# Kernel tuning notes

Hardware: AMD Instinct MI355X
Metric: run time of the kernel (lower is better)

## Reference

```python
import jax, jax.numpy as jnp
import numpy as np

B, L = 8, 512
D_MODEL, N_HEADS, N_LAYERS = 768, 12, 12
D_HEAD = D_MODEL // N_HEADS
D_FF = 4 * D_MODEL
NUM_LABELS = 1000
PATCH_DIM = 16 * 16 * 3
EPS = 1e-6


def setup_inputs() -> dict:
    key = jax.random.key(0)
    ks = jax.random.split(key, 24)
    d = D_MODEL

    def w(k, shape, fan_in):
        return (jax.random.normal(k, shape, jnp.float32) / np.sqrt(fan_in)).astype(jnp.float32)

    return {
        'patch': jax.random.normal(ks[0], (B, L, PATCH_DIM), jnp.float32),
        'box': jax.random.uniform(ks[1], (B, L, 4), jnp.float32),
        'patch_W': w(ks[2], (PATCH_DIM, d), PATCH_DIM),
        'patch_b': jnp.zeros((d,), jnp.float32),
        'box_W': w(ks[3], (d, d), d),
        'box_b': jnp.zeros((d,), jnp.float32),
        'Wq': w(ks[4], (N_LAYERS, d, d), d),
        'Wk': w(ks[5], (N_LAYERS, d, d), d),
        'Wv': w(ks[6], (N_LAYERS, d, d), d),
        'Wo': w(ks[7], (N_LAYERS, d, d), d),
        'attn_norm_w': jnp.ones((N_LAYERS, d), jnp.float32),
        'gate_W': w(ks[8], (N_LAYERS, d, D_FF), d),
        'hidden_W': w(ks[9], (N_LAYERS, d, D_FF), d),
        'ffn_out_W': w(ks[10], (N_LAYERS, D_FF, d), D_FF),
        'ffn_norm_w': jnp.ones((N_LAYERS, d), jnp.float32),
        'reward_norm_w': jnp.ones((d,), jnp.float32),
        'reward_W': w(ks[11], (d, 2), d),
        'reward_b': jnp.zeros((2,), jnp.float32),
        'label_norm_w': jnp.ones((d,), jnp.float32),
        'label_W': w(ks[12], (d, NUM_LABELS), d),
        'label_b': jnp.zeros((NUM_LABELS,), jnp.float32),
        'box_norm_w': jnp.ones((d,), jnp.float32),
        'boxh_W': w(ks[13], (d, 4), d),
        'boxh_b': jnp.zeros((4,), jnp.float32),
    }


def _rmsnorm(x, wgt):
    return x * jax.lax.rsqrt(jnp.mean(x * x, axis=-1, keepdims=True) + EPS) * wgt


def _rope(x, cos, sin):
    # x: [b, n, l, dh]; consecutive pairs form complex numbers (view_as_complex)
    xr, xi = x[..., 0::2], x[..., 1::2]
    out_r = xr * cos - xi * sin
    out_i = xr * sin + xi * cos
    return jnp.stack((out_r, out_i), axis=-1).reshape(x.shape)


def _forward(patch, box, patch_W, patch_b, box_W, box_b, Wq, Wk, Wv, Wo,
             attn_norm_w, gate_W, hidden_W, ffn_out_W, ffn_norm_w,
             reward_norm_w, reward_W, reward_b, label_norm_w, label_W, label_b,
             box_norm_w, boxh_W, boxh_b):
    b, l, _ = patch.shape
    d = D_MODEL
    # StackedSinusoidalEmbedding(d_model, 4): d_stack = d/4, theta over d_stack/2 freqs
    d_stack = d // 4
    theta_box = 1.0 / (10000.0 ** (2.0 * jnp.arange(d_stack // 2, dtype=jnp.float32) / d_stack))
    ang = box[..., None] * theta_box  # [b, l, 4, d_stack/2]
    box_sin = jnp.stack((jnp.cos(ang), jnp.sin(ang)), axis=-1).reshape(b, l, d)

    x = (patch @ patch_W + patch_b) + (box_sin @ box_W + box_b)

    # RoPE tables and causal mask (constants)
    theta = 1.0 / (10000.0 ** (2.0 * jnp.arange(D_HEAD // 2, dtype=jnp.float32) / D_HEAD))
    pos_ang = jnp.arange(l, dtype=jnp.float32)[:, None] * theta  # [l, dh/2]
    cos, sin = jnp.cos(pos_ang), jnp.sin(pos_ang)
    mask = jnp.triu(jnp.full((l, l), -jnp.inf, dtype=jnp.float32), 1)
    scale = jnp.float32(np.sqrt(D_HEAD))

    def block(h, p):
        wq, wk, wv, wo, anw, gw, hw, ow, fnw = p
        hn = _rmsnorm(h, anw)
        q = (hn @ wq).reshape(b, l, N_HEADS, D_HEAD).transpose(0, 2, 1, 3)
        k = (hn @ wk).reshape(b, l, N_HEADS, D_HEAD).transpose(0, 2, 1, 3)
        v = (hn @ wv).reshape(b, l, N_HEADS, D_HEAD).transpose(0, 2, 1, 3)
        scores = jnp.einsum('bnld,bnmd->bnlm', _rope(q, cos, sin), _rope(k, cos, sin)) / scale
        attn = jax.nn.softmax(scores + mask, axis=-1)
        o = jnp.einsum('bnlm,bnmd->bnld', attn, v).transpose(0, 2, 1, 3).reshape(b, l, d)
        h = h + o @ wo
        hn = _rmsnorm(h, fnw)
        h = h + (jax.nn.silu(hn @ gw) * (hn @ hw)) @ ow
        return h, None

    x, _ = jax.lax.scan(block, x, (Wq, Wk, Wv, Wo, attn_norm_w, gate_W, hidden_W, ffn_out_W, ffn_norm_w))

    reward = _rmsnorm(x, reward_norm_w) @ reward_W + reward_b
    label = _rmsnorm(x, label_norm_w) @ label_W + label_b
    box_out = _rmsnorm(x, box_norm_w) @ boxh_W + boxh_b
    return reward, label, box_out


def reference(patch, box, patch_W, patch_b, box_W, box_b, Wq, Wk, Wv, Wo,
              attn_norm_w, gate_W, hidden_W, ffn_out_W, ffn_norm_w,
              reward_norm_w, reward_W, reward_b, label_norm_w, label_W, label_b,
              box_norm_w, boxh_W, boxh_b):
    return _forward(patch, box, patch_W, patch_b, box_W, box_b, Wq, Wk, Wv, Wo,
                    attn_norm_w, gate_W, hidden_W, ffn_out_W, ffn_norm_w,
                    reward_norm_w, reward_W, reward_b, label_norm_w, label_W, label_b,
                    box_norm_w, boxh_W, boxh_b)
```

## Files before the change

### kernel.cpp

```cpp
#include <hip/hip_runtime.h>
#include <math.h>
#include <type_traits>

#define B_   8
#define L_   512
#define MTOK 4096
#define D_   768
#define NH_  12
#define DH_  64
#define DFF_ 3072
#define NL_  12

typedef unsigned short u16;
typedef __attribute__((ext_vector_type(4))) float f32x4;
typedef __attribute__((ext_vector_type(8))) short i16x8;
typedef __attribute__((ext_vector_type(8))) __bf16 b16x8;

template <typename A, typename = void>
struct PickFrag { using type = i16x8; };
template <typename A>
struct PickFrag<A, std::void_t<decltype(__builtin_amdgcn_mfma_f32_16x16x32_bf16(
    std::declval<A>(), std::declval<A>(), std::declval<f32x4>(), 0, 0, 0))>> {
  using type = A;
};
using frag_t = typename PickFrag<b16x8>::type;

#if __has_builtin(__builtin_amdgcn_global_load_lds)
#define HAS_GLDS 1
#else
#define HAS_GLDS 0
#endif

__device__ inline u16 f2bf(float f) {
    unsigned u = __float_as_uint(f);
    unsigned r = u + 0x7fffu + ((u >> 16) & 1u);
    return (u16)(r >> 16);
}
__device__ inline float bf2f(u16 b) { return __uint_as_float(((unsigned)b) << 16); }

__device__ inline void bar_raw() {
    asm volatile("" ::: "memory");
    __builtin_amdgcn_s_barrier();
    asm volatile("" ::: "memory");
}

__device__ inline int swz8(int row, int c8) { return c8 ^ ((row & 7) << 3); }

__global__ void k_box_sin(u16* __restrict__ emb, const float* __restrict__ box) {
    int idx = blockIdx.x * blockDim.x + threadIdx.x;
    if (idx >= MTOK * D_) return;
    int t = idx / D_, d = idx % D_;
    int c = d / 192, r = d % 192, j = r >> 1;
    float theta = __expf(-(float)j * (9.210340371976184f / 96.0f));
    float ang = box[t * 4 + c] * theta;
    emb[(size_t)t * 1536 + 768 + d] = f2bf((r & 1) ? sinf(ang) : cosf(ang));
}

__global__ void k_cast(u16* __restrict__ emb, const float* __restrict__ in, int n4) {
    int i = blockIdx.x * blockDim.x + threadIdx.x;
    if (i >= n4) return;
    int t = i / 192, c4 = (i % 192) * 4;
    float4 v = *reinterpret_cast<const float4*>(in + (size_t)t * 768 + c4);
    unsigned lo = (unsigned)f2bf(v.x) | ((unsigned)f2bf(v.y) << 16);
    unsigned hi = (unsigned)f2bf(v.z) | ((unsigned)f2bf(v.w) << 16);
    *reinterpret_cast<uint2*>(emb + (size_t)t * 1536 + c4) = make_uint2(lo, hi);
}

__global__ void k_addb(float* __restrict__ dst, const float* __restrict__ a,
                       const float* __restrict__ b) {
    int i = blockIdx.x * blockDim.x + threadIdx.x;
    if (i < D_) dst[i] = a[i] + b[i];
}

__global__ __launch_bounds__(256) void k_convT(u16* __restrict__ dst,
                                               const float* __restrict__ src,
                                               int K, int N, int ld, int rs,
                                               int ro, int co) {
    __shared__ float t[32][33];
    int bn = blockIdx.x * 32;
    int bk = blockIdx.y * 32;
    int tx = threadIdx.x % 32, ty = threadIdx.x / 32;
    #pragma unroll
    for (int i = 0; i < 4; ++i) {
        int k = bk + ty + i * 8;
        int n = bn + tx;
        t[ty + i * 8][tx] = (n < N) ? src[(size_t)k * N + n] : 0.0f;
    }
    __syncthreads();
    #pragma unroll
    for (int i = 0; i < 4; ++i) {
        int n = bn + ty + i * 8;
        int k = bk + tx;
        dst[(size_t)(n * rs + ro) * ld + co + k] = f2bf(t[tx][ty + i * 8]);
    }
}


__global__ __launch_bounds__(256) void k_convT128(u16* __restrict__ dst,
                                                  const float* __restrict__ src,
                                                  int K, int N) {
    __shared__ float ts[32][130];
    const float* s = src + (size_t)blockIdx.z * K * N;
    u16* d = dst + (size_t)blockIdx.z * K * N;
    int bn = blockIdx.x * 32, bk = blockIdx.y * 128;
    int t = threadIdx.x, rn = t & 31, kr = t >> 5;
    #pragma unroll
    for (int p = 0; p < 16; ++p) {
        int k = p * 8 + kr;
        ts[rn][k] = s[(size_t)(bk + k) * N + bn + rn];
    }
    __syncthreads();
    int n = t >> 3, kc = (t & 7) * 16;
    u16 tmp[16];
    #pragma unroll
    for (int j = 0; j < 16; ++j) tmp[j] = f2bf(ts[n][kc + j]);
    u16* dp = &d[(size_t)(bn + n) * K + bk + kc];
    *reinterpret_cast<uint4*>(dp)     = *reinterpret_cast<uint4*>(tmp);
    *reinterpret_cast<uint4*>(dp + 8) = *reinterpret_cast<uint4*>(tmp + 8);
}

__global__ __launch_bounds__(256) void k_convT128_qkv(u16* __restrict__ dst,
                                                      const float* __restrict__ s0,
                                                      const float* __restrict__ s1,
                                                      const float* __restrict__ s2) {
    __shared__ float ts[32][130];
    int ly = blockIdx.z / 3, which = blockIdx.z % 3;
    const float* s = (which == 0 ? s0 : (which == 1 ? s1 : s2)) + (size_t)ly * 768 * 768;
    u16* d = dst + ((size_t)ly * 3 + which) * 768 * 768;
    int bn = blockIdx.x * 32, bk = blockIdx.y * 128;
    int t = threadIdx.x, rn = t & 31, kr = t >> 5;
    #pragma unroll
    for (int p = 0; p < 16; ++p) {
        int k = p * 8 + kr;
        ts[rn][k] = s[(size_t)(bk + k) * 768 + bn + rn];
    }
    __syncthreads();
    int n = t >> 3, kc = (t & 7) * 16;
    u16 tmp[16];
    #pragma unroll
    for (int j = 0; j < 16; ++j) tmp[j] = f2bf(ts[n][kc + j]);
    u16* dp = &d[(size_t)(bn + n) * 768 + bk + kc];
    *reinterpret_cast<uint4*>(dp)     = *reinterpret_cast<uint4*>(tmp);
    *reinterpret_cast<uint4*>(dp + 8) = *reinterpret_cast<uint4*>(tmp + 8);
}

__global__ __launch_bounds__(256) void k_convT128_gh(u16* __restrict__ dst,
                                                     const float* __restrict__ g,
                                                     const float* __restrict__ h) {
    __shared__ float ts[32][130];
    int ly = blockIdx.z >> 1, which = blockIdx.z & 1;
    const float* s = (which ? h : g) + (size_t)ly * 768 * 3072;
    u16* d = dst + (size_t)ly * 6144 * 768;
    int bn = blockIdx.x * 32, bk = blockIdx.y * 128;
    int t = threadIdx.x, rn = t & 31, kr = t >> 5;
    #pragma unroll
    for (int p = 0; p < 16; ++p) {
        int k = p * 8 + kr;
        ts[rn][k] = s[(size_t)(bk + k) * 3072 + bn + rn];
    }
    __syncthreads();
    int n = t >> 3, kc = (t & 7) * 16;
    int ng = bn + n;
    int row = ((ng >> 4) << 5) + (ng & 15) + which * 16;
    u16 tmp[16];
    #pragma unroll
    for (int j = 0; j < 16; ++j) tmp[j] = f2bf(ts[n][kc + j]);
    u16* dp = &d[(size_t)row * 768 + bk + kc];
    *reinterpret_cast<uint4*>(dp)     = *reinterpret_cast<uint4*>(tmp);
    *reinterpret_cast<uint4*>(dp + 8) = *reinterpret_cast<uint4*>(tmp + 8);
}

__global__ __launch_bounds__(256) void k_rmsnorm(u16* __restrict__ out,
                                                 const float* __restrict__ in,
                                                 const float* __restrict__ w) {
    int t = blockIdx.x;
    const float* x = in + (size_t)t * D_;
    float ss = 0.f;
    for (int i = threadIdx.x; i < D_; i += 256) { float v = x[i]; ss += v * v; }
    for (int off = 32; off > 0; off >>= 1) ss += __shfl_down(ss, off);
    __shared__ float red[4];
    int wid = threadIdx.x >> 6, lane = threadIdx.x & 63;
    if (lane == 0) red[wid] = ss;
    __syncthreads();
    float tot = red[0] + red[1] + red[2] + red[3];
    float inv = rsqrtf(tot / (float)D_ + 1e-6f);
    for (int i = threadIdx.x; i < D_; i += 256)
        out[(size_t)t * D_ + i] = f2bf(x[i] * inv * w[i]);
}

template <int S>
__global__ __launch_bounds__(256) void k_fused_rr(float* __restrict__ h,
                                                  const float* __restrict__ part,
                                                  u16* __restrict__ hn,
                                                  const float* __restrict__ w) {
    int t = blockIdx.x;
    size_t base = (size_t)t * D_;
    float x[3];
    float ss = 0.f;
    #pragma unroll
    for (int c = 0; c < 3; ++c) {
        int i = threadIdx.x + c * 256;
        float v = h[base + i];
        #pragma unroll
        for (int s = 0; s < S; ++s)
            v += part[(size_t)s * MTOK * D_ + base + i];
        x[c] = v;
        h[base + i] = v;
        ss += v * v;
    }
    for (int off = 32; off > 0; off >>= 1) ss += __shfl_down(ss, off);
    __shared__ float red[4];
    int wid = threadIdx.x >> 6, lane = threadIdx.x & 63;
    if (lane == 0) red[wid] = ss;
    __syncthreads();
    float tot = red[0] + red[1] + red[2] + red[3];
    float inv = rsqrtf(tot / (float)D_ + 1e-6f);
    #pragma unroll
    for (int c = 0; c < 3; ++c) {
        int i = threadIdx.x + c * 256;
        hn[base + i] = f2bf(x[c] * inv * w[i]);
    }
}

__global__ void k_rope_tab(float* __restrict__ tab) {
    int idx = blockIdx.x * blockDim.x + threadIdx.x;
    if (idx >= L_ * 32) return;
    int l = idx >> 5, j = idx & 31;
    float theta = __expf(-(float)j * (9.210340371976184f / 32.0f));
    float s, c;
    sincosf((float)l * theta, &s, &c);
    tab[idx * 2] = c;
    tab[idx * 2 + 1] = s;
}

template <int MODE>
__global__ __launch_bounds__(256) void k_gemm_bf16(void* __restrict__ Cp,
                                                   const u16* __restrict__ A,
                                                   const u16* __restrict__ BT,
                                                   const float* __restrict__ bias,
                                                   int K, int Nout, int ldC) {
    __shared__ u16 smem[16384];
    int tid = threadIdx.x;
    int wid = tid >> 6, lane = tid & 63;

    int nx = gridDim.x, ny = gridDim.y, nz = gridDim.z;
    int bid = ((blockIdx.z * ny) + blockIdx.y) * nx + blockIdx.x;
    int nwg = nx * ny * nz;
    int cpx = nwg >> 3;
    int swz = (bid & 7) * cpx + (bid >> 3);
    int sk  = swz / (nx * ny);
    int rem = swz % (nx * ny);
    int by = rem / nx, bx = rem % nx;
    int row0 = by * 128, col0 = bx * 128;
    int wr = wid >> 1, wc = wid & 1;

    int Klen = K / nz;
    int kbeg = sk * Klen;

    int c0 = wid * 128 + lane;
    int c1 = c0 + 64;
    int r0 = c0 >> 2, kc0 = (c0 & 3) * 8;
    int r1 = c1 >> 2, kc1 = (c1 & 3) * 8;
    const u16* gA0 = A  + (size_t)(row0 + r0) * K + kbeg + kc0;
    const u16* gA1 = A  + (size_t)(row0 + r1) * K + kbeg + kc1;
    const u16* gB0 = BT + (size_t)(col0 + r0) * K + kbeg + kc0;
    const u16* gB1 = BT + (size_t)(col0 + r1) * K + kbeg + kc1;

    auto stage = [&](int buf, int kt) {
        u16* Asb = smem + buf * 4096;
        u16* Bsb = smem + 8192 + buf * 4096;
#if HAS_GLDS
        __builtin_amdgcn_global_load_lds(
            (const __attribute__((address_space(1))) void*)(gA0 + kt),
            (__attribute__((address_space(3))) void*)&Asb[c0 * 8], 16, 0, 0);
        __builtin_amdgcn_global_load_lds(
            (const __attribute__((address_space(1))) void*)(gA1 + kt),
            (__attribute__((address_space(3))) void*)&Asb[c1 * 8], 16, 0, 0);
        __builtin_amdgcn_global_load_lds(
            (const __attribute__((address_space(1))) void*)(gB0 + kt),
            (__attribute__((address_space(3))) void*)&Bsb[c0 * 8], 16, 0, 0);
        __builtin_amdgcn_global_load_lds(
            (const __attribute__((address_space(1))) void*)(gB1 + kt),
            (__attribute__((address_space(3))) void*)&Bsb[c1 * 8], 16, 0, 0);
#else
        *reinterpret_cast<uint4*>(&Asb[c0 * 8]) = *reinterpret_cast<const uint4*>(gA0 + kt);
        *reinterpret_cast<uint4*>(&Asb[c1 * 8]) = *reinterpret_cast<const uint4*>(gA1 + kt);
        *reinterpret_cast<uint4*>(&Bsb[c0 * 8]) = *reinterpret_cast<const uint4*>(gB0 + kt);
        *reinterpret_cast<uint4*>(&Bsb[c1 * 8]) = *reinterpret_cast<const uint4*>(gB1 + kt);
#endif
    };

    f32x4 acc[4][4] = {};
    int lrow = lane & 15, lk = (lane >> 4) * 8;

    stage(0, 0);
    int cur = 0;
    for (int kt = 0; kt < Klen; kt += 32) {
        bool has_next = (kt + 32 < Klen);
        if (has_next) stage(cur ^ 1, kt + 32);
        if (has_next) asm volatile("s_waitcnt vmcnt(4) lgkmcnt(0)" ::: "memory");
        else          asm volatile("s_waitcnt vmcnt(0) lgkmcnt(0)" ::: "memory");
        __builtin_amdgcn_sched_barrier(0);
        bar_raw();
        const u16* Asb = smem + cur * 4096;
        const u16* Bsb = smem + 8192 + cur * 4096;
        frag_t af[4], bfr[4];
        #pragma unroll
        for (int m = 0; m < 4; ++m)
            af[m] = *reinterpret_cast<const frag_t*>(&Asb[(wr * 64 + m * 16 + lrow) * 32 + lk]);
        #pragma unroll
        for (int n = 0; n < 4; ++n)
            bfr[n] = *reinterpret_cast<const frag_t*>(&Bsb[(wc * 64 + n * 16 + lrow) * 32 + lk]);
        #pragma unroll
        for (int m = 0; m < 4; ++m)
            #pragma unroll
            for (int n = 0; n < 4; ++n)
                acc[m][n] = __builtin_amdgcn_mfma_f32_16x16x32_bf16(af[m], bfr[n], acc[m][n], 0, 0, 0);
        bar_raw();
        cur ^= 1;
    }

    int lcol = lane & 15, rb = (lane >> 4) * 4;

    if (MODE == 6) {
        u16* qkvh = (u16*)Cp;
        const float* tab = bias;
        if (col0 >= 1536) {
            int head_base = (col0 - 1536) >> 6;
            int bb = row0 >> 9;
            int l0 = row0 & 511;
            #pragma unroll
            for (int pass = 0; pass < 2; ++pass) {
                if (wc == pass) {
                    #pragma unroll
                    for (int m = 0; m < 4; ++m) {
                        #pragma unroll
                        for (int n = 0; n < 4; ++n) {
                            int dl = n * 16 + lcol;
                            int rl = wr * 64 + m * 16 + rb;
                            u16 tmp[4];
                            #pragma unroll
                            for (int e = 0; e < 4; ++e) tmp[e] = f2bf(acc[m][n][e]);
                            *reinterpret_cast<uint2*>(&smem[dl * 136 + rl]) =
                                *reinterpret_cast<uint2*>(tmp);
                        }
                    }
                }
                __syncthreads();
                int head = head_base + pass;
                size_t vbase = (size_t)2 * MTOK * 768 +
                               ((size_t)(bb * NH_ + head) * 64) * 512;
                #pragma unroll
                for (int it = 0; it < 4; ++it) {
                    int dd = it * 16 + (tid >> 4);
                    int rr = (tid & 15) * 8;
                    uint4 v4 = *reinterpret_cast<const uint4*>(&smem[dd * 136 + rr]);
                    *reinterpret_cast<uint4*>(&qkvh[vbase + (size_t)dd * 512 + l0 + rr]) = v4;
                }
                __syncthreads();
            }
        } else {
            int sec = col0 / 768;
            float qscale = (sec == 0) ? 0.125f : 1.0f;
            #pragma unroll
            for (int m = 0; m < 4; ++m) {
                #pragma unroll
                for (int n = 0; n < 4; ++n) {
                    int col = col0 + wc * 64 + n * 16 + lcol;
                    int head = (col % 768) >> 6;
                    int d = col & 63;
                    #pragma unroll
                    for (int e = 0; e < 4; ++e) {
                        int row = row0 + wr * 64 + m * 16 + rb + e;
                        int bb = row >> 9, l = row & 511;
                        float v = acc[m][n][e];
                        float p = __shfl_xor(v, 1);
                        float2 cs = *reinterpret_cast<const float2*>(
                            tab + ((size_t)l * 32 + (d >> 1)) * 2);
                        float r = (d & 1) ? (p * cs.y + v * cs.x)
                                          : (v * cs.x - p * cs.y);
                        r *= qscale;
                        qkvh[(size_t)sec * MTOK * 768 +
                             ((size_t)(bb * NH_ + head) * 512 + l) * 64 + d] = f2bf(r);
                    }
                }
            }
        }
        return;
    }

    if (MODE == 5) {
        #pragma unroll
        for (int m = 0; m < 4; ++m) {
            #pragma unroll
            for (int np = 0; np < 2; ++np) {
                int ocol = (col0 >> 1) + wc * 32 + np * 16 + lcol;
                #pragma unroll
                for (int e = 0; e < 4; ++e) {
                    int row = row0 + wr * 64 + m * 16 + rb + e;
                    float g = acc[m][2 * np][e], hv = acc[m][2 * np + 1][e];
                    float s = g / (1.0f + __expf(-g));
                    ((u16*)Cp)[(size_t)row * ldC + ocol] = f2bf(s * hv);
                }
            }
        }
        return;
    }

    float* Cpart = (MODE == 4)
        ? ((float*)Cp + (size_t)sk * (size_t)(ny * 128) * ldC) : (float*)Cp;
    #pragma unroll
    for (int m = 0; m < 4; ++m) {
        #pragma unroll
        for (int n = 0; n < 4; ++n) {
            int col = col0 + wc * 64 + n * 16 + lcol;
            if (col >= Nout) continue;
            #pragma unroll
            for (int e = 0; e < 4; ++e) {
                int row = row0 + wr * 64 + m * 16 + rb + e;
                float v = acc[m][n][e];
                size_t off = (size_t)row * ldC + col;
                if (MODE == 0) {
                    if (bias) v += bias[col];
                    ((float*)Cp)[off] = v;
                } else if (MODE == 3) {
                    ((u16*)Cp)[off] = f2bf(v);
                } else if (MODE == 4) {
                    Cpart[off] = v;
                }
            }
        }
    }
}

__global__ __launch_bounds__(256) void k_attn3(u16* __restrict__ o,
                                               const u16* __restrict__ qh,
                                               const u16* __restrict__ kh,
                                               const u16* __restrict__ vT) {
    int bh = blockIdx.x, qb = blockIdx.y;
    int b = bh / NH_, hh = bh % NH_;
    int tid = threadIdx.x, wid = tid >> 6, lane = tid & 63;
    __shared__ u16 Qs[64][72], Ps[64][72];
    __shared__ u16 Ks[64 * 64], Vs[64 * 64];

    #pragma unroll
    for (int i = 0; i < 2; ++i) {
        int idx = tid + i * 256;
        int r = idx >> 3, c8 = (idx & 7) * 8;
        uint4 v4 = *reinterpret_cast<const uint4*>(
            qh + ((size_t)bh * L_ + qb * 64 + r) * 64 + c8);
        *reinterpret_cast<uint4*>(&Qs[r][c8]) = v4;
    }
    __syncthreads();

    int lr = lane & 15, lg = lane >> 4;
    frag_t aq[2];
    #pragma unroll
    for (int kd = 0; kd < 2; ++kd)
        aq[kd] = *reinterpret_cast<const frag_t*>(&Qs[wid * 16 + lr][kd * 32 + lg * 8]);

    int sr0 = tid >> 3, sc8 = (tid & 7) * 8;
    int sr1 = sr0 + 32;

    f32x4 accO[4] = {};
    float M[4], S[4];
    #pragma unroll
    for (int e = 0; e < 4; ++e) { M[e] = -INFINITY; S[e] = 0.f; }

    uint4 kreg0 = *reinterpret_cast<const uint4*>(kh + ((size_t)bh * L_ + sr0) * 64 + sc8);
    uint4 kreg1 = *reinterpret_cast<const uint4*>(kh + ((size_t)bh * L_ + sr1) * 64 + sc8);
    uint4 vreg0 = *reinterpret_cast<const uint4*>(vT + ((size_t)bh * 64 + sr0) * L_ + sc8);
    uint4 vreg1 = *reinterpret_cast<const uint4*>(vT + ((size_t)bh * 64 + sr1) * L_ + sc8);

    for (int kb = 0; kb <= qb; ++kb) {
        __syncthreads();
        *reinterpret_cast<uint4*>(&Ks[sr0 * 64 + swz8(sr0, sc8)]) = kreg0;
        *reinterpret_cast<uint4*>(&Ks[sr1 * 64 + swz8(sr1, sc8)]) = kreg1;
        *reinterpret_cast<uint4*>(&Vs[sr0 * 64 + swz8(sr0, sc8)]) = vreg0;
        *reinterpret_cast<uint4*>(&Vs[sr1 * 64 + swz8(sr1, sc8)]) = vreg1;
        __syncthreads();
        if (kb < qb) {
            int nb = (kb + 1) * 64;
            kreg0 = *reinterpret_cast<const uint4*>(kh + ((size_t)bh * L_ + nb + sr0) * 64 + sc8);
            kreg1 = *reinterpret_cast<const uint4*>(kh + ((size_t)bh * L_ + nb + sr1) * 64 + sc8);
            vreg0 = *reinterpret_cast<const uint4*>(vT + ((size_t)bh * 64 + sr0) * L_ + nb + sc8);
            vreg1 = *reinterpret_cast<const uint4*>(vT + ((size_t)bh * 64 + sr1) * L_ + nb + sc8);
        }

        f32x4 sv[4];
        __builtin_amdgcn_s_setprio(1);
        #pragma unroll
        for (int ct = 0; ct < 4; ++ct) {
            int krow = ct * 16 + lr;
            frag_t bk0 = *reinterpret_cast<const frag_t*>(&Ks[krow * 64 + swz8(krow, lg * 8)]);
            frag_t bk1 = *reinterpret_cast<const frag_t*>(&Ks[krow * 64 + swz8(krow, 32 + lg * 8)]);
            f32x4 z = {0.f, 0.f, 0.f, 0.f};
            z = __builtin_amdgcn_mfma_f32_16x16x32_bf16(aq[0], bk0, z, 0, 0, 0);
            sv[ct] = __builtin_amdgcn_mfma_f32_16x16x32_bf16(aq[1], bk1, z, 0, 0, 0);
        }
        __builtin_amdgcn_s_setprio(0);

        bool diag = (kb == qb);
        float esc[4];
        #pragma unroll
        for (int e = 0; e < 4; ++e) {
            int qg = qb * 64 + wid * 16 + lg * 4 + e;
            float mx = -1e30f;
            #pragma unroll
            for (int ct = 0; ct < 4; ++ct) {
                float s = sv[ct][e];
                if (diag && (kb * 64 + ct * 16 + lr > qg)) s = -1e30f;
                sv[ct][e] = s;
                mx = fmaxf(mx, s);
            }
            #pragma unroll
            for (int msk = 8; msk; msk >>= 1) mx = fmaxf(mx, __shfl_xor(mx, msk));
            float newM = fmaxf(M[e], mx);
            float ps = 0.f;
            #pragma unroll
            for (int ct = 0; ct < 4; ++ct) {
                float p = __expf(sv[ct][e] - newM);
                sv[ct][e] = p;
                ps += p;
            }
            #pragma unroll
            for (int msk = 8; msk; msk >>= 1) ps += __shfl_xor(ps, msk);
            esc[e] = __expf(M[e] - newM);
            S[e] = S[e] * esc[e] + ps;
            M[e] = newM;
        }
        #pragma unroll
        for (int dt = 0; dt < 4; ++dt)
            #pragma unroll
            for (int e = 0; e < 4; ++e) accO[dt][e] *= esc[e];

        #pragma unroll
        for (int ct = 0; ct < 4; ++ct)
            #pragma unroll
            for (int e = 0; e < 4; ++e)
                Ps[wid * 16 + lg * 4 + e][ct * 16 + lr] = f2bf(sv[ct][e]);

        frag_t pa0 = *reinterpret_cast<const frag_t*>(&Ps[wid * 16 + lr][lg * 8]);
        frag_t pa1 = *reinterpret_cast<const frag_t*>(&Ps[wid * 16 + lr][32 + lg * 8]);
        __builtin_amdgcn_s_setprio(1);
        #pragma unroll
        for (int dt = 0; dt < 4; ++dt) {
            int vrow = dt * 16 + lr;
            frag_t bv0 = *reinterpret_cast<const frag_t*>(&Vs[vrow * 64 + swz8(vrow, lg * 8)]);
            frag_t bv1 = *reinterpret_cast<const frag_t*>(&Vs[vrow * 64 + swz8(vrow, 32 + lg * 8)]);
            accO[dt] = __builtin_amdgcn_mfma_f32_16x16x32_bf16(pa0, bv0, accO[dt], 0, 0, 0);
            accO[dt] = __builtin_amdgcn_mfma_f32_16x16x32_bf16(pa1, bv1, accO[dt], 0, 0, 0);
        }
        __builtin_amdgcn_s_setprio(0);
    }

    #pragma unroll
    for (int dt = 0; dt < 4; ++dt) {
        #pragma unroll
        for (int e = 0; e < 4; ++e) {
            int row = b * L_ + qb * 64 + wid * 16 + lg * 4 + e;
            o[(size_t)row * D_ + hh * 64 + dt * 16 + lr] = f2bf(accO[dt][e] / S[e]);
        }
    }
}

__global__ __launch_bounds__(256) void k_heads3(float* __restrict__ out_reward,
                                                float* __restrict__ out_box,
                                                const float* __restrict__ h,
                                                const float* __restrict__ rnw,
                                                const float* __restrict__ rW,
                                                const float* __restrict__ rb,
                                                const float* __restrict__ bnw,
                                                const float* __restrict__ bW,
                                                const float* __restrict__ bb) {
    int t = blockIdx.x;
    size_t base = (size_t)t * D_;
    float x[3];
    float ss = 0.f;
    #pragma unroll
    for (int c = 0; c < 3; ++c) {
        int i = threadIdx.x + c * 256;
        x[c] = h[base + i];
        ss += x[c] * x[c];
    }
    for (int off = 32; off > 0; off >>= 1) ss += __shfl_down(ss, off);
    __shared__ float red[4];
    int wid = threadIdx.x >> 6, lane = threadIdx.x & 63;
    if (lane == 0) red[wid] = ss;
    __syncthreads();
    float inv = rsqrtf((red[0] + red[1] + red[2] + red[3]) / (float)D_ + 1e-6f);

    float a[6] = {};
    #pragma unroll
    for (int c = 0; c < 3; ++c) {
        int i = threadIdx.x + c * 256;
        float xr = x[c] * inv;
        float xw = xr * rnw[i];
        a[0] += xw * rW[i * 2];
        a[1] += xw * rW[i * 2 + 1];
        float xb = xr * bnw[i];
        #pragma unroll
        for (int j = 0; j < 4; ++j) a[2 + j] += xb * bW[i * 4 + j];
    }
    #pragma unroll
    for (int j = 0; j < 6; ++j)
        for (int off = 32; off > 0; off >>= 1) a[j] += __shfl_down(a[j], off);
    __shared__ float red2[4][6];
    if (lane == 0)
        #pragma unroll
        for (int j = 0; j < 6; ++j) red2[wid][j] = a[j];
    __syncthreads();
    if (threadIdx.x < 6) {
        float s = red2[0][threadIdx.x] + red2[1][threadIdx.x] +
                  red2[2][threadIdx.x] + red2[3][threadIdx.x];
        if (threadIdx.x < 2) out_reward[(size_t)t * 2 + threadIdx.x] = s + rb[threadIdx.x];
        else                 out_box[(size_t)t * 4 + threadIdx.x - 2] = s + bb[threadIdx.x - 2];
    }
}

extern "C" void kernel_launch(void* const* d_in, const int* in_sizes, int n_in,
                              void* d_out, int out_size, void* d_ws, size_t ws_size,
                              hipStream_t stream) {
    const float* patch        = (const float*)d_in[0];
    const float* box          = (const float*)d_in[1];
    const float* patch_W      = (const float*)d_in[2];
    const float* patch_b      = (const float*)d_in[3];
    const float* box_W        = (const float*)d_in[4];
    const float* box_b        = (const float*)d_in[5];
    const float* Wq           = (const float*)d_in[6];
    const float* Wk           = (const float*)d_in[7];
    const float* Wv           = (const float*)d_in[8];
    const float* Wo           = (const float*)d_in[9];
    const float* attn_norm_w  = (const float*)d_in[10];
    const float* gate_W       = (const float*)d_in[11];
    const float* hidden_W     = (const float*)d_in[12];
    const float* ffn_out_W    = (const float*)d_in[13];
    const float* ffn_norm_w   = (const float*)d_in[14];
    const float* reward_norm_w= (const float*)d_in[15];
    const float* reward_W     = (const float*)d_in[16];
    const float* reward_b     = (const float*)d_in[17];
    const float* label_norm_w = (const float*)d_in[18];
    const float* label_W      = (const float*)d_in[19];
    const float* label_b      = (const float*)d_in[20];
    const float* box_norm_w   = (const float*)d_in[21];
    const float* boxh_W       = (const float*)d_in[22];
    const float* boxh_b       = (const float*)d_in[23];

    char* w = (char*)d_ws;
    auto alloc = [&](size_t bytes) { char* p = w; w += (bytes + 255) & ~(size_t)255; return p; };

    u16*  wqkv_a = (u16*)alloc((size_t)NL_ * 2304 * 768 * 2);
    u16*  wo_a   = (u16*)alloc((size_t)NL_ * 768 * 768 * 2);
    u16*  wgh_a  = (u16*)alloc((size_t)NL_ * 6144 * 768 * 2);
    u16*  wfo_a  = (u16*)alloc((size_t)NL_ * 768 * 3072 * 2);
    u16*  wcat   = (u16*)alloc((size_t)768 * 1536 * 2);
    u16*  wlab   = (u16*)alloc((size_t)1024 * 768 * 2);
    float* bias_c= (float*)alloc((size_t)768 * 4);
    u16*  emb    = (u16*)alloc((size_t)MTOK * 1536 * 2);
    float* h     = (float*)alloc((size_t)MTOK * D_ * 4);
    u16*  hn_bf  = (u16*)alloc((size_t)MTOK * D_ * 2);
    u16*  qkvh   = (u16*)alloc((size_t)MTOK * 2304 * 2);
    float* tab   = (float*)alloc((size_t)L_ * 32 * 2 * 4);
    u16*  o_bf   = (u16*)alloc((size_t)MTOK * D_ * 2);
    u16*  ga_bf  = (u16*)alloc((size_t)MTOK * DFF_ * 2);
    float* part  = (float*)alloc((size_t)4 * MTOK * D_ * 4);

    u16* qh = qkvh;
    u16* kh = qkvh + (size_t)MTOK * 768;
    u16* vT = qkvh + (size_t)2 * MTOK * 768;

    dim3 blk(256);

    k_convT<<<dim3(24, 24), blk, 0, stream>>>(wcat, patch_W, 768, 768, 1536, 1, 0, 0);
    k_convT<<<dim3(24, 24), blk, 0, stream>>>(wcat, box_W,   768, 768, 1536, 1, 0, 768);
    k_convT<<<dim3(32, 24), blk, 0, stream>>>(wlab, label_W, 768, 1000, 768, 1, 0, 0);
    k_addb<<<3, blk, 0, stream>>>(bias_c, patch_b, box_b);
    k_rope_tab<<<(L_ * 32 + 255) / 256, blk, 0, stream>>>(tab);
    k_convT128_qkv<<<dim3(24, 6, 36), blk, 0, stream>>>(wqkv_a, Wq, Wk, Wv);
    k_convT128<<<dim3(24, 6, 12), blk, 0, stream>>>(wo_a, Wo, 768, 768);
    k_convT128_gh<<<dim3(96, 6, 24), blk, 0, stream>>>(wgh_a, gate_W, hidden_W);
    k_convT128<<<dim3(24, 24, 12), blk, 0, stream>>>(wfo_a, ffn_out_W, 3072, 768);
    k_cast<<<(MTOK * 768 / 4 + 255) / 256, blk, 0, stream>>>(emb, patch, MTOK * 768 / 4);
    k_box_sin<<<(MTOK * D_ + 255) / 256, blk, 0, stream>>>(emb, box);

    k_gemm_bf16<0><<<dim3(6, 32), blk, 0, stream>>>(h, emb, wcat, bias_c, 1536, 768, 768);
    k_rmsnorm<<<MTOK, blk, 0, stream>>>(hn_bf, h, attn_norm_w);

    for (int ly = 0; ly < NL_; ++ly) {
        const u16* wqkv = wqkv_a + (size_t)ly * 2304 * 768;
        const u16* wo_l = wo_a   + (size_t)ly * 768 * 768;
        const u16* wgh  = wgh_a  + (size_t)ly * 6144 * 768;
        const u16* wfo  = wfo_a  + (size_t)ly * 768 * 3072;
        const float* fnw = ffn_norm_w + (size_t)ly * D_;
        const float* nxt = (ly + 1 < NL_) ? attn_norm_w + (size_t)(ly + 1) * D_
                                          : label_norm_w;

        k_gemm_bf16<6><<<dim3(18, 32), blk, 0, stream>>>(qkvh, hn_bf, wqkv, tab, 768, 2304, 2304);
        k_attn3<<<dim3(96, 8), blk, 0, stream>>>(o_bf, qh, kh, vT);
        k_gemm_bf16<4><<<dim3(6, 32, 2), blk, 0, stream>>>(part, o_bf, wo_l, nullptr, 768, 768, 768);
        k_fused_rr<2><<<MTOK, blk, 0, stream>>>(h, part, hn_bf, fnw);

        k_gemm_bf16<5><<<dim3(48, 32), blk, 0, stream>>>(ga_bf, hn_bf, wgh, nullptr, 768, 6144, 3072);
        k_gemm_bf16<4><<<dim3(6, 32, 4), blk, 0, stream>>>(part, ga_bf, wfo, nullptr, 3072, 768, 768);
        k_fused_rr<4><<<MTOK, blk, 0, stream>>>(h, part, hn_bf, nxt);
    }

    float* out_reward = (float*)d_out;
    float* out_label  = out_reward + (size_t)MTOK * 2;
    float* out_box    = out_label + (size_t)MTOK * 1000;

    k_gemm_bf16<0><<<dim3(8, 32), blk, 0, stream>>>(out_label, hn_bf, wlab, label_b, 768, 1000, 1000);
    k_heads3<<<MTOK, blk, 0, stream>>>(out_reward, out_box, h,
                                       reward_norm_w, reward_W, reward_b,
                                       box_norm_w, boxh_W, boxh_b);
}
```

Baseline: 2.319 ms.

## Add 256x256-tile 512-thread GEMM for fused gate/hidden SwiGLU projection

Replaces the 128x128-tile, 256-thread GEMM used for the fused gate/hidden projection with a dedicated kernel using 256x256 tiles, 8 waves, and 8x4 MFMA fragments per wave. Larger tiles raise arithmetic intensity and cut global/LDS traffic per FLOP. In exchange the grid drops to 384 blocks, which is lower parallelism on a large-CU device, and register pressure rises from 128 accumulator floats per thread. Also pads the transpose-kernel shared tiles from 130 to 131 columns to reduce bank conflicts, and factors the global-to-LDS load into a helper.

```diff
diff --git a/kernel.cpp b/kernel.cpp
--- a/kernel.cpp
+++ b/kernel.cpp
@@ -46,6 +46,16 @@
 
 __device__ inline int swz8(int row, int c8) { return c8 ^ ((row & 7) << 3); }
 
+__device__ inline void glds16(const u16* g, u16* l) {
+#if HAS_GLDS
+    __builtin_amdgcn_global_load_lds(
+        (const __attribute__((address_space(1))) void*)g,
+        (__attribute__((address_space(3))) void*)l, 16, 0, 0);
+#else
+    *reinterpret_cast<uint4*>(l) = *reinterpret_cast<const uint4*>(g);
+#endif
+}
+
 __global__ void k_box_sin(u16* __restrict__ emb, const float* __restrict__ box) {
     int idx = blockIdx.x * blockDim.x + threadIdx.x;
     if (idx >= MTOK * D_) return;
@@ -99,7 +109,7 @@
 __global__ __launch_bounds__(256) void k_convT128(u16* __restrict__ dst,
                                                   const float* __restrict__ src,
                                                   int K, int N) {
-    __shared__ float ts[32][130];
+    __shared__ float ts[32][131];
     const float* s = src + (size_t)blockIdx.z * K * N;
     u16* d = dst + (size_t)blockIdx.z * K * N;
     int bn = blockIdx.x * 32, bk = blockIdx.y * 128;
@@ -123,7 +133,7 @@
                                                       const float* __restrict__ s0,
                                                       const float* __restrict__ s1,
                                                       const float* __restrict__ s2) {
-    __shared__ float ts[32][130];
+    __shared__ float ts[32][131];
     int ly = blockIdx.z / 3, which = blockIdx.z % 3;
     const float* s = (which == 0 ? s0 : (which == 1 ? s1 : s2)) + (size_t)ly * 768 * 768;
     u16* d = dst + ((size_t)ly * 3 + which) * 768 * 768;
@@ -147,7 +157,7 @@
 __global__ __launch_bounds__(256) void k_convT128_gh(u16* __restrict__ dst,
                                                      const float* __restrict__ g,
                                                      const float* __restrict__ h) {
-    __shared__ float ts[32][130];
+    __shared__ float ts[32][131];
     int ly = blockIdx.z >> 1, which = blockIdx.z & 1;
     const float* s = (which ? h : g) + (size_t)ly * 768 * 3072;
     u16* d = dst + (size_t)ly * 6144 * 768;
@@ -233,6 +243,88 @@
     tab[idx * 2 + 1] = s;
 }
 
+__global__ __launch_bounds__(512) void k_gemm512_gh(u16* __restrict__ Cp,
+                                                    const u16* __restrict__ A,
+                                                    const u16* __restrict__ BT,
+                                                    int K, int ldC) {
+    __shared__ u16 smem[32768];
+    int tid = threadIdx.x;
+    int wid = tid >> 6, lane = tid & 63;
+
+    int nx = gridDim.x, ny = gridDim.y;
+    int bid = blockIdx.y * nx + blockIdx.x;
+    int nwg = nx * ny;
+    int cpx = nwg >> 3;
+    int swzb = (bid & 7) * cpx + (bid >> 3);
+    int by = swzb / nx, bx = swzb % nx;
+    int row0 = by * 256, col0 = bx * 256;
+    int wr = wid >> 2, wcn = wid & 3;
+
+    int c0 = tid, c1 = tid + 512;
+    int r0 = c0 >> 2, r1 = c1 >> 2;
+    int gsrc = (((tid & 3) ^ ((tid >> 3) & 3)) << 3);
+    const u16* gA0 = A  + (size_t)(row0 + r0) * K + gsrc;
+    const u16* gA1 = A  + (size_t)(row0 + r1) * K + gsrc;
+    const u16* gB0 = BT + (size_t)(col0 + r0) * K + gsrc;
+    const u16* gB1 = BT + (size_t)(col0 + r1) * K + gsrc;
+
+    auto stage = [&](int buf, int kt) {
+        u16* Asb = smem + buf * 8192;
+        u16* Bsb = smem + 16384 + buf * 8192;
+        glds16(gA0 + kt, &Asb[c0 * 8]);
+        glds16(gA1 + kt, &Asb[c1 * 8]);
+        glds16(gB0 + kt, &Bsb[c0 * 8]);
+        glds16(gB1 + kt, &Bsb[c1 * 8]);
+    };
+
+    f32x4 acc[8][4] = {};
+    int lr = lane & 15, lg = lane >> 4;
+    int lk = (((lg ^ ((lr >> 1) & 3))) << 3);
+
+    stage(0, 0);
+    int cur = 0;
+    for (int kt = 0; kt < K; kt += 32) {
+        bool has_next = (kt + 32 < K);
+        if (has_next) stage(cur ^ 1, kt + 32);
+        if (has_next) asm volatile("s_waitcnt vmcnt(4) lgkmcnt(0)" ::: "memory");
+        else          asm volatile("s_waitcnt vmcnt(0) lgkmcnt(0)" ::: "memory");
+        __builtin_amdgcn_sched_barrier(0);
+        bar_raw();
+        const u16* Asb = smem + cur * 8192;
+        const u16* Bsb = smem + 16384 + cur * 8192;
+        frag_t af[8], bfr[4];
+        #pragma unroll
+        for (int m = 0; m < 8; ++m)
+            af[m] = *reinterpret_cast<const frag_t*>(&Asb[(wr * 128 + m * 16 + lr) * 32 + lk]);
+        #pragma unroll
+        for (int n = 0; n < 4; ++n)
+            bfr[n] = *reinterpret_cast<const frag_t*>(&Bsb[(wcn * 64 + n * 16 + lr) * 32 + lk]);
+        #pragma unroll
+        for (int m = 0; m < 8; ++m)
+            #pragma unroll
+            for (int n = 0; n < 4; ++n)
+                acc[m][n] = __builtin_amdgcn_mfma_f32_16x16x32_bf16(af[m], bfr[n], acc[m][n], 0, 0, 0);
+        bar_raw();
+        cur ^= 1;
+    }
+
+    int lcol = lane & 15, rb = (lane >> 4) * 4;
+    #pragma unroll
+    for (int m = 0; m < 8; ++m) {
+        #pragma unroll
+        for (int np = 0; np < 2; ++np) {
+            int ocol = (col0 >> 1) + wcn * 32 + np * 16 + lcol;
+            #pragma unroll
+            for (int e = 0; e < 4; ++e) {
+                int row = row0 + wr * 128 + m * 16 + rb + e;
+                float g = acc[m][2 * np][e], hv = acc[m][2 * np + 1][e];
+                float s = g / (1.0f + __expf(-g));
+                Cp[(size_t)row * ldC + ocol] = f2bf(s * hv);
+            }
+        }
+    }
+}
+
 template <int MODE>
 __global__ __launch_bounds__(256) void k_gemm_bf16(void* __restrict__ Cp,
                                                    const u16* __restrict__ A,
@@ -269,25 +361,10 @@
     auto stage = [&](int buf, int kt) {
         u16* Asb = smem + buf * 4096;
         u16* Bsb = smem + 8192 + buf * 4096;
-#if HAS_GLDS
-        __builtin_amdgcn_global_load_lds(
-            (const __attribute__((address_space(1))) void*)(gA0 + kt),
-            (__attribute__((address_space(3))) void*)&Asb[c0 * 8], 16, 0, 0);
-        __builtin_amdgcn_global_load_lds(
-            (const __attribute__((address_space(1))) void*)(gA1 + kt),
-            (__attribute__((address_space(3))) void*)&Asb[c1 * 8], 16, 0, 0);
-        __builtin_amdgcn_global_load_lds(
-            (const __attribute__((address_space(1))) void*)(gB0 + kt),
-            (__attribute__((address_space(3))) void*)&Bsb[c0 * 8], 16, 0, 0);
-        __builtin_amdgcn_global_load_lds(
-            (const __attribute__((address_space(1))) void*)(gB1 + kt),
-            (__attribute__((address_space(3))) void*)&Bsb[c1 * 8], 16, 0, 0);
-#else
-        *reinterpret_cast<uint4*>(&Asb[c0 * 8]) = *reinterpret_cast<const uint4*>(gA0 + kt);
-        *reinterpret_cast<uint4*>(&Asb[c1 * 8]) = *reinterpret_cast<const uint4*>(gA1 + kt);
-        *reinterpret_cast<uint4*>(&Bsb[c0 * 8]) = *reinterpret_cast<const uint4*>(gB0 + kt);
-        *reinterpret_cast<uint4*>(&Bsb[c1 * 8]) = *reinterpret_cast<const uint4*>(gB1 + kt);
-#endif
+        glds16(gA0 + kt, &Asb[c0 * 8]);
+        glds16(gA1 + kt, &Asb[c1 * 8]);
+        glds16(gB0 + kt, &Bsb[c0 * 8]);
+        glds16(gB1 + kt, &Bsb[c1 * 8]);
     };
 
     f32x4 acc[4][4] = {};
@@ -389,24 +466,6 @@
         return;
     }
 
-    if (MODE == 5) {
-        #pragma unroll
-        for (int m = 0; m < 4; ++m) {
-            #pragma unroll
-            for (int np = 0; np < 2; ++np) {
-                int ocol = (col0 >> 1) + wc * 32 + np * 16 + lcol;
-                #pragma unroll
-                for (int e = 0; e < 4; ++e) {
-                    int row = row0 + wr * 64 + m * 16 + rb + e;
-                    float g = acc[m][2 * np][e], hv = acc[m][2 * np + 1][e];
-                    float s = g / (1.0f + __expf(-g));
-                    ((u16*)Cp)[(size_t)row * ldC + ocol] = f2bf(s * hv);
-                }
-            }
-        }
-        return;
-    }
-
     float* Cpart = (MODE == 4)
         ? ((float*)Cp + (size_t)sk * (size_t)(ny * 128) * ldC) : (float*)Cp;
     #pragma unroll
@@ -700,7 +759,7 @@
         k_gemm_bf16<4><<<dim3(6, 32, 2), blk, 0, stream>>>(part, o_bf, wo_l, nullptr, 768, 768, 768);
         k_fused_rr<2><<<MTOK, blk, 0, stream>>>(h, part, hn_bf, fnw);
 
-        k_gemm_bf16<5><<<dim3(48, 32), blk, 0, stream>>>(ga_bf, hn_bf, wgh, nullptr, 768, 6144, 3072);
+        k_gemm512_gh<<<dim3(24, 16), dim3(512), 0, stream>>>(ga_bf, hn_bf, wgh, 768, 3072);
         k_gemm_bf16<4><<<dim3(6, 32, 4), blk, 0, stream>>>(part, ga_bf, wfo, nullptr, 3072, 768, 768);
         k_fused_rr<4><<<MTOK, blk, 0, stream>>>(h, part, hn_bf, nxt);
     }
```

After: 2.305 ms. About the same (-0.6%).
